# Kernel optimization log

Hardware: AMD Instinct MI355X
Metric: run time of the kernel (lower is better)

The kernel has to match this reference:

```python
import jax, jax.numpy as jnp
import numpy as np

D_MODEL = 512
N_HEADS = 8
D_KV = 64
INNER = N_HEADS * D_KV
NUM_BUCKETS = 32
MAX_DISTANCE = 128
LN_EPS = 1e-6


def _relative_position_bucket(rel, num_buckets=NUM_BUCKETS, max_distance=MAX_DISTANCE):
    # bidirectional T5 bucketing
    nb = num_buckets // 2
    buckets = (rel > 0).astype(jnp.int32) * nb
    rel = jnp.abs(rel)
    max_exact = nb // 2
    is_small = rel < max_exact
    relf = jnp.maximum(rel.astype(jnp.float32), 1.0)  # guard log(0)
    large = max_exact + (
        jnp.log(relf / max_exact) / np.log(max_distance / max_exact) * (nb - max_exact)
    ).astype(jnp.int32)
    large = jnp.minimum(large, nb - 1)
    return buckets + jnp.where(is_small, rel, large)


def t5_layer_norm(x, weight, eps=LN_EPS):
    # T5 LayerNorm: no mean subtraction, no bias
    var = jnp.mean(jnp.square(x), axis=-1, keepdims=True)
    return x * jax.lax.rsqrt(var + eps) * weight


def compute_position_bias(rel_bias_table, q_len, k_len):
    ctx = jnp.arange(q_len)[:, None]
    mem = jnp.arange(k_len)[None, :]
    buckets = _relative_position_bucket(mem - ctx)  # [q, k]
    bias = rel_bias_table[buckets]                  # [q, k, H]
    return jnp.transpose(bias, (2, 0, 1))[None]     # [1, H, q, k]


def setup_inputs() -> dict:
    key = jax.random.key(0)
    ks = jax.random.split(key, 8)
    N, S = 8, 2048
    s = 1.0 / np.sqrt(D_MODEL)
    return {
        "hidden_states": jax.random.normal(ks[0], (N, S, D_MODEL), jnp.float32),
        "ln_weight": jnp.ones((D_MODEL,), jnp.float32),
        "wq": jax.random.normal(ks[1], (D_MODEL, INNER), jnp.float32) * s,
        "wk": jax.random.normal(ks[2], (D_MODEL, INNER), jnp.float32) * s,
        "wv": jax.random.normal(ks[3], (D_MODEL, INNER), jnp.float32) * s,
        "wo": jax.random.normal(ks[4], (INNER, D_MODEL), jnp.float32) * s,
        "rel_bias_table": jax.random.normal(ks[5], (NUM_BUCKETS, N_HEADS), jnp.float32) * 0.1,
        "seq_idx2graph_idx": jax.random.randint(ks[6], (8,), 0, 8, jnp.int64) if jax.config.jax_enable_x64 else jax.random.randint(ks[6], (8,), 0, 8, jnp.int32),
    }


def reference(hidden_states, ln_weight, wq, wk, wv, wo, rel_bias_table, seq_idx2graph_idx):
    N, S, _ = hidden_states.shape
    normed = t5_layer_norm(hidden_states, ln_weight)

    # T5Attention (no 1/sqrt(d) scaling in T5)
    q = jnp.einsum("nsd,de->nse", normed, wq).reshape(N, S, N_HEADS, D_KV)
    k = jnp.einsum("nsd,de->nse", normed, wk).reshape(N, S, N_HEADS, D_KV)
    v = jnp.einsum("nsd,de->nse", normed, wv).reshape(N, S, N_HEADS, D_KV)

    position_bias = compute_position_bias(rel_bias_table, S, S)  # [1,H,S,S]
    scores = jnp.einsum("nqhd,nkhd->nhqk", q, k) + position_bias
    attn = jax.nn.softmax(scores, axis=-1)
    ctx = jnp.einsum("nhqk,nkhd->nqhd", attn, v).reshape(N, S, INNER)
    attn_out = jnp.einsum("nse,ed->nsd", ctx, wo)

    # residual (dropout is identity in eval)
    hidden = hidden_states + attn_out
    remain_node_idx = jnp.arange(seq_idx2graph_idx.shape[0])
    return hidden, position_bias, remain_node_idx
```

## Files before the change

kernel.cpp:

```cpp
#include <hip/hip_runtime.h>
#include <hip/hip_bf16.h>
#include <math.h>

typedef __bf16 bf16;
typedef bf16 bf16x8 __attribute__((ext_vector_type(8)));
typedef bf16 bf16x4 __attribute__((ext_vector_type(4)));
typedef float f32x2 __attribute__((ext_vector_type(2)));
typedef float f32x4 __attribute__((ext_vector_type(4)));
typedef float f32x16 __attribute__((ext_vector_type(16)));

#define MFMA16(a, b, c) __builtin_amdgcn_mfma_f32_16x16x32_bf16(a, b, c, 0, 0, 0)
#define MFMA32(a, b, c) __builtin_amdgcn_mfma_f32_32x32x16_bf16(a, b, c, 0, 0, 0)
#define LOG2E 1.4426950408889634f
#define NEG_SHIFT -40.0f

__device__ __forceinline__ void glds16(const bf16* g, bf16* l) {
  __builtin_amdgcn_global_load_lds(
      (const __attribute__((address_space(1))) void*)g,
      (__attribute__((address_space(3))) void*)l, 16, 0, 0);
}

__device__ inline unsigned pkbf(float a, float b) {
  union { bf16 h; unsigned short u; } ca, cb;
  ca.h = (bf16)a;
  cb.h = (bf16)b;
  return (unsigned)ca.u | ((unsigned)cb.u << 16);
}

__device__ __forceinline__ void pl32swap(unsigned& a, unsigned& b) {
  asm("v_permlane32_swap_b32 %0, %1" : "+v"(a), "+v"(b));
}

__device__ inline float t5bias(const float* __restrict__ table, int h, int x) {
  if (x > 4094) return 0.f;
  int rel = x - 2047;
  int bucket = (rel > 0) ? 16 : 0;
  int ar = rel < 0 ? -rel : rel;
  int v;
  if (ar < 8) {
    v = ar;
  } else {
    double tt = log((double)ar / 8.0) / log(16.0) * 8.0;
    int lg = 8 + (int)tt;
    v = lg < 15 ? lg : 15;
  }
  return table[(bucket + v) * 8 + h];
}

__global__ __launch_bounds__(256) void prep_kernel(
    const float* __restrict__ hidden, const float* __restrict__ ln_w,
    const float* __restrict__ wq, const float* __restrict__ wk,
    const float* __restrict__ wv, const float* __restrict__ wo,
    const float* __restrict__ table, bf16* __restrict__ normed,
    float* __restrict__ lut, float4* __restrict__ lutq,
    float* __restrict__ out_remain, bf16* __restrict__ wt_qkv,
    bf16* __restrict__ wt_o) {
  __shared__ float tile[32][33];
  int bid = blockIdx.x;
  int t = threadIdx.x;
  if (bid < 4096) {
    int row = bid * 4 + (t >> 6);
    int lane = t & 63;
    const float4* xr = (const float4*)(hidden + (size_t)row * 512);
    float4 a = xr[lane];
    float4 b = xr[lane + 64];
    float s = a.x * a.x + a.y * a.y + a.z * a.z + a.w * a.w +
              b.x * b.x + b.y * b.y + b.z * b.z + b.w * b.w;
#pragma unroll
    for (int off = 32; off > 0; off >>= 1) s += __shfl_down(s, off, 64);
    float tot = __shfl(s, 0, 64);
    float rscale = rsqrtf(tot * (1.0f / 512.0f) + 1e-6f);
    float4 w0 = *(const float4*)(ln_w + 4 * lane);
    float4 w1 = *(const float4*)(ln_w + 256 + 4 * lane);
    bf16x4 o0, o1;
    o0[0] = (bf16)(a.x * rscale * w0.x);
    o0[1] = (bf16)(a.y * rscale * w0.y);
    o0[2] = (bf16)(a.z * rscale * w0.z);
    o0[3] = (bf16)(a.w * rscale * w0.w);
    o1[0] = (bf16)(b.x * rscale * w1.x);
    o1[1] = (bf16)(b.y * rscale * w1.y);
    o1[2] = (bf16)(b.z * rscale * w1.z);
    o1[3] = (bf16)(b.w * rscale * w1.w);
    *(bf16x4*)(normed + (size_t)row * 512 + 4 * lane) = o0;
    *(bf16x4*)(normed + (size_t)row * 512 + 256 + 4 * lane) = o1;
  } else if (bid < 4224) {
    int i = (bid - 4096) * 256 + t;
    int h = i >> 12;
    int d = i & 4095;
    lut[(size_t)h * 4096 + d] = t5bias(table, h, d);
    if (i < 8) out_remain[i] = (float)i;
  } else if (bid < 5248) {
    int bid2 = bid - 4224;
    int mat = bid2 >> 8;
    int rem = bid2 & 255;
    int e0 = (rem & 15) * 32;
    int k0 = (rem >> 4) * 32;
    int tx = t & 31, ty = t >> 5;
    const float* W = (mat == 0) ? wq : (mat == 1) ? wk : (mat == 2) ? wv : wo;
#pragma unroll
    for (int j = 0; j < 32; j += 8)
      tile[ty + j][tx] = W[(size_t)(k0 + ty + j) * 512 + e0 + tx];
    __syncthreads();
    bf16* dst = (mat < 3) ? (wt_qkv + (size_t)mat * 512 * 512) : wt_o;
#pragma unroll
    for (int j = 0; j < 32; j += 8)
      dst[(size_t)(e0 + ty + j) * 512 + k0 + tx] = (bf16)tile[tx][ty + j];
  } else {
    int i = (bid - 5248) * 256 + t;
    int h = i >> 12;
    int d = i & 4095;
    float4 o;
    o.x = t5bias(table, h, d) * LOG2E + NEG_SHIFT;
    o.y = t5bias(table, h, d + 1) * LOG2E + NEG_SHIFT;
    o.z = t5bias(table, h, d + 2) * LOG2E + NEG_SHIFT;
    o.w = t5bias(table, h, d + 3) * LOG2E + NEG_SHIFT;
    lutq[(size_t)h * 4096 + d] = o;
  }
}

__global__ __launch_bounds__(256) void qkv_gemm(
    const bf16* __restrict__ normed, const bf16* __restrict__ wt,
    bf16* __restrict__ qb, bf16* __restrict__ kb, bf16* __restrict__ vtb) {
  __shared__ __align__(16) char smem[19456];
  bf16* As = (bf16*)smem;
  bf16* Bs = (bf16*)(smem + 8192);
  int t = threadIdx.x;
  int wave = t >> 6, lane = t & 63;
  int quad = lane >> 4, lc = lane & 15;
  int wm = wave >> 1, wn = wave & 1;
  int m0 = blockIdx.x * 128, n0 = blockIdx.y * 128;

  f32x4 acc[4][4];
#pragma unroll
  for (int i = 0; i < 4; i++)
#pragma unroll
    for (int j = 0; j < 4; j++) acc[i][j] = (f32x4){0.f, 0.f, 0.f, 0.f};

  int rw = lane >> 2;
  int c8 = (lane & 3) * 8;
  const bf16* gA = normed + (size_t)(m0 + wave * 32 + rw) * 512 + c8;
  const bf16* gB = wt + (size_t)(n0 + wave * 32 + rw) * 512 + c8;
  bf16* lA = As + wave * 1024;
  bf16* lB = Bs + wave * 1024;

  for (int kt = 0; kt < 16; ++kt) {
    int k0 = kt * 32;
    __syncthreads();
    glds16(gA + k0, lA);
    glds16(gA + 16 * 512 + k0, lA + 512);
    glds16(gB + k0, lB);
    glds16(gB + 16 * 512 + k0, lB + 512);
    __syncthreads();
    bf16x8 af[4], bfr[4];
#pragma unroll
    for (int i = 0; i < 4; i++)
      af[i] = *(const bf16x8*)&As[(wm * 64 + i * 16 + lc) * 32 + quad * 8];
#pragma unroll
    for (int j = 0; j < 4; j++)
      bfr[j] = *(const bf16x8*)&Bs[(wn * 64 + j * 16 + lc) * 32 + quad * 8];
#pragma unroll
    for (int i = 0; i < 4; i++)
#pragma unroll
      for (int j = 0; j < 4; j++)
        acc[i][j] = MFMA16(af[i], bfr[j], acc[i][j]);
  }

  __syncthreads();
  int mat = n0 >> 9;
  int e_base = (n0 & 511) + wn * 64;
  int hh = e_base >> 6;
  int grow0 = m0 + wm * 64;
  int nbi = grow0 >> 11, sbase = grow0 & 2047;

  if (mat == 2) {
    bf16* dv = vtb + ((size_t)(nbi * 8 + hh) * 64) * 2048;
#pragma unroll
    for (int i = 0; i < 4; i++) {
      int s = sbase + i * 16 + quad * 4;
#pragma unroll
      for (int j = 0; j < 4; j++) {
        int d = j * 16 + lc;
        bf16x4 o4;
#pragma unroll
        for (int r = 0; r < 4; r++) o4[r] = (bf16)acc[i][j][r];
        *(bf16x4*)(dv + (size_t)d * 2048 + s) = o4;
      }
    }
  } else {
    float qsc = (mat == 0) ? LOG2E : 1.0f;
    bf16* dst0 = (mat == 0) ? qb : kb;
    bf16* dst = dst0 + (((size_t)nbi * 8 + hh) * 2048 + sbase) * 64;
    bf16* Cw = (bf16*)smem + wave * 2432;
#pragma unroll
    for (int p = 0; p < 2; ++p) {
#pragma unroll
      for (int i2 = 0; i2 < 2; ++i2) {
#pragma unroll
        for (int j = 0; j < 4; ++j)
#pragma unroll
          for (int r = 0; r < 4; ++r)
            Cw[(i2 * 16 + quad * 4 + r) * 76 + j * 16 + lc] =
                (bf16)(acc[2 * p + i2][j][r] * qsc);
      }
#pragma unroll
      for (int c = 0; c < 4; ++c) {
        bf16x8 vch =
            *(const bf16x8*)&Cw[(c * 8 + (lane >> 3)) * 76 + (lane & 7) * 8];
        *(bf16x8*)(dst + (size_t)(p * 32 + c * 8 + (lane >> 3)) * 64 +
                   (lane & 7) * 8) = vch;
      }
    }
  }
}

#define LDB4(SV, G, V4)       \
  {                           \
    float4 _b = (V4);         \
    SV[4 * (G) + 0] = _b.x;   \
    SV[4 * (G) + 1] = _b.y;   \
    SV[4 * (G) + 2] = _b.z;   \
    SV[4 * (G) + 3] = _b.w;   \
  }

#define BODY(RB, WB, PF)                                                     \
  {                                                                          \
    if (PF) {                                                                \
      kv0 = *(const bf16x8*)(kpc);                                           \
      kv1 = *(const bf16x8*)(kpc + 8);                                       \
      vv0 = *(const bf16x8*)(vpc);                                           \
      vv1 = *(const bf16x8*)(vpc + 8);                                       \
    }                                                                        \
    _Pragma("unroll") for (int mi = 0; mi < 2; mi++) {                       \
      __builtin_amdgcn_s_setprio(1);                                         \
      _Pragma("unroll") for (int c = 0; c < 4; c++) {                        \
        bf16x8 kf = *(const bf16x8*)&Ks[RB][mi * 32 + l31][c * 16 + hi * 8]; \
        st[mi] = MFMA32(kf, Qf[c], st[mi]);                                  \
      }                                                                      \
      __builtin_amdgcn_s_setprio(0);                                         \
      unsigned D[8];                                                         \
      _Pragma("unroll") for (int g = 0; g < 4; g++) {                        \
        _Pragma("unroll") for (int e = 0; e < 4; e++)                        \
            st[mi][4 * g + e] = __builtin_amdgcn_exp2f(st[mi][4 * g + e]);   \
        lsA += (f32x2){st[mi][4 * g + 0], st[mi][4 * g + 1]};                \
        lsB += (f32x2){st[mi][4 * g + 2], st[mi][4 * g + 3]};                \
        D[2 * g] = pkbf(st[mi][4 * g + 0], st[mi][4 * g + 1]);               \
        D[2 * g + 1] = pkbf(st[mi][4 * g + 2], st[mi][4 * g + 3]);           \
      }                                                                      \
      if (PF) {         \
        LDB4(st[mi], 0, bpn[mi * 32 + 0]);                                   \
        LDB4(st[mi], 1, bpn[mi * 32 + 8]);                                   \
        LDB4(st[mi], 2, bpn[mi * 32 + 16]);                                  \
        LDB4(st[mi], 3, bpn[mi * 32 + 24]);                                  \
      }                                                                      \
      pl32swap(D[0], D[2]);                                                  \
      pl32swap(D[1], D[3]);                                                  \
      pl32swap(D[4], D[6]);                                                  \
      pl32swap(D[5], D[7]);                                                  \
      _Pragma("unroll") for (int kk = 0; kk < 2; kk++) {                     \
        int kc = 2 * mi + kk;                                                \
        union { uint4 u; bf16x8 v; } cv;                                     \
        cv.u = make_uint4(D[4 * kk + 0], D[4 * kk + 1], D[4 * kk + 2],       \
                          D[4 * kk + 3]);                                    \
        bf16x8 pf = cv.v;                                                    \
        __builtin_amdgcn_s_setprio(1);                                       \
        _Pragma("unroll") for (int md = 0; md < 2; md++) {                   \
          bf16x8 vf =                                                        \
              *(const bf16x8*)&Vs[RB][md * 32 + l31][kc * 16 + hi * 8];      \
          O[md] = MFMA32(vf, pf, O[md]);                                     \
        }                                                                    \
        __builtin_amdgcn_s_setprio(0);                                       \
      }                                                                      \
    }                                                                        \
    if (PF) {                                                                \
      *(bf16x8*)&Ks[WB][srow][scol] = kv0;                                   \
      *(bf16x8*)&Ks[WB][srow][scol + 8] = kv1;                               \
      *(bf16x8*)&Vs[WB][srow][scol] = vv0;                                   \
      *(bf16x8*)&Vs[WB][srow][scol + 8] = vv1;                               \
      kpc += 4096;                                                           \
      vpc += 64;                                                             \
      bpn += 64;                                                             \
    }                                                                        \
    __syncthreads();                                                         \
  }

__global__ __launch_bounds__(256, 4) void attn_kernel(
    const bf16* __restrict__ qg, const bf16* __restrict__ kg,
    const bf16* __restrict__ vtg, const float4* __restrict__ lutq,
    bf16* __restrict__ ctx) {
  __shared__ bf16 Ks[2][64][72];
  __shared__ bf16 Vs[2][64][72];
  int t = threadIdx.x;

  int id = blockIdx.x;
  int xcd = id & 7, slot = id >> 3;
  int bh = xcd * 8 + (slot >> 4);
  int qt = slot & 15;
  int n = bh >> 3, h = bh & 7;
  int q0 = qt * 128;

  int wave = t >> 6, lane = t & 63;
  int l31 = lane & 31, hi = lane >> 5;
  int q = q0 + wave * 32 + l31;

  const float4* bp = lutq + (size_t)h * 4096 + (2047 + 4 * hi - q);

  const bf16* qp = qg + ((size_t)bh * 2048 + q) * 64;
  bf16x8 Qf[4];
#pragma unroll
  for (int c = 0; c < 4; c++) Qf[c] = *(const bf16x8*)(qp + c * 16 + hi * 8);

  f32x16 O[2];
#pragma unroll
  for (int i = 0; i < 2; i++)
#pragma unroll
    for (int e = 0; e < 16; e++) O[i][e] = 0.f;
  f32x2 lsA = {0.f, 0.f}, lsB = {0.f, 0.f};

  int srow = t >> 2, scol = (t & 3) * 16;
  const bf16* kp = kg + (size_t)bh * 2048 * 64 + srow * 64 + scol;
  const bf16* vp = vtg + (size_t)bh * 64 * 2048 + (size_t)srow * 2048 + scol;

  bf16x8 kv0 = *(const bf16x8*)(kp);
  bf16x8 kv1 = *(const bf16x8*)(kp + 8);
  bf16x8 vv0 = *(const bf16x8*)(vp);
  bf16x8 vv1 = *(const bf16x8*)(vp + 8);
  *(bf16x8*)&Ks[0][srow][scol] = kv0;
  *(bf16x8*)&Ks[0][srow][scol + 8] = kv1;
  *(bf16x8*)&Vs[0][srow][scol] = vv0;
  *(bf16x8*)&Vs[0][srow][scol + 8] = vv1;
  f32x16 st[2];
  LDB4(st[0], 0, bp[0]);
  LDB4(st[0], 1, bp[8]);
  LDB4(st[0], 2, bp[16]);
  LDB4(st[0], 3, bp[24]);
  LDB4(st[1], 0, bp[32]);
  LDB4(st[1], 1, bp[40]);
  LDB4(st[1], 2, bp[48]);
  LDB4(st[1], 3, bp[56]);
  const bf16* kpc = kp + 4096;
  const bf16* vpc = vp + 64;
  const float4* bpn = bp + 64;
  __syncthreads();

#pragma unroll 1
  for (int it = 0; it < 15; ++it) {
    BODY(0, 1, 1)
    BODY(1, 0, 1)
  }
  BODY(0, 1, 1)
  BODY(1, 0, 0)

  float l_run = lsA.x + lsA.y + lsB.x + lsB.y;
  l_run += __shfl_xor(l_run, 32, 64);
  float inv = 1.0f / l_run;
  bf16* cp = ctx + ((size_t)n * 2048 + q) * 512 + h * 64;
#pragma unroll
  for (int md = 0; md < 2; md++)
#pragma unroll
    for (int g = 0; g < 4; g++) {
      bf16x4 o4;
#pragma unroll
      for (int e = 0; e < 4; e++) o4[e] = (bf16)(O[md][4 * g + e] * inv);
      *(bf16x4*)(cp + md * 32 + 8 * g + hi * 4) = o4;
    }
}

__global__ __launch_bounds__(256) void oproj_gemm(
    const bf16* __restrict__ ctx, const bf16* __restrict__ wt_o,
    const float* __restrict__ hidden, float* __restrict__ out,
    const float* __restrict__ lut, float* __restrict__ bias_out) {
  __shared__ __align__(16) char smem[16384];
  int t = threadIdx.x;
  int bid = blockIdx.x;

  if (bid >= 512) {
    int bb = bid - 512;
#pragma unroll
    for (int j = 0; j < 4; ++j) {
      size_t i = ((size_t)bb * 1024 + j * 256 + t) * 4;
      int h = (int)(i >> 22);
      int q = (int)((i >> 11) & 2047);
      int k = (int)(i & 2047);
      const float* lh = lut + (size_t)h * 4096 + (2047 - q);
      float4 v = {lh[k], lh[k + 1], lh[k + 2], lh[k + 3]};
      *(float4*)(bias_out + i) = v;
    }
    return;
  }

  bf16* As = (bf16*)smem;
  bf16* Bs = (bf16*)(smem + 8192);
  int wave = t >> 6, lane = t & 63;
  int quad = lane >> 4, lc = lane & 15;
  int wm = wave >> 1, wn = wave & 1;
  int m0 = (bid & 127) * 128, n0 = (bid >> 7) * 128;

  f32x4 acc[4][4];
#pragma unroll
  for (int i = 0; i < 4; i++)
#pragma unroll
    for (int j = 0; j < 4; j++) acc[i][j] = (f32x4){0.f, 0.f, 0.f, 0.f};

  int rw = lane >> 2;
  int c8 = (lane & 3) * 8;
  const bf16* gA = ctx + (size_t)(m0 + wave * 32 + rw) * 512 + c8;
  const bf16* gB = wt_o + (size_t)(n0 + wave * 32 + rw) * 512 + c8;
  bf16* lA = As + wave * 1024;
  bf16* lB = Bs + wave * 1024;

  for (int kt = 0; kt < 16; ++kt) {
    int k0 = kt * 32;
    __syncthreads();
    glds16(gA + k0, lA);
    glds16(gA + 16 * 512 + k0, lA + 512);
    glds16(gB + k0, lB);
    glds16(gB + 16 * 512 + k0, lB + 512);
    __syncthreads();
    bf16x8 af[4], bfr[4];
#pragma unroll
    for (int i = 0; i < 4; i++)
      af[i] = *(const bf16x8*)&As[(wm * 64 + i * 16 + lc) * 32 + quad * 8];
#pragma unroll
    for (int j = 0; j < 4; j++)
      bfr[j] = *(const bf16x8*)&Bs[(wn * 64 + j * 16 + lc) * 32 + quad * 8];
#pragma unroll
    for (int i = 0; i < 4; i++)
#pragma unroll
      for (int j = 0; j < 4; j++)
        acc[i][j] = MFMA16(af[i], bfr[j], acc[i][j]);
  }

#pragma unroll
  for (int i = 0; i < 4; i++) {
#pragma unroll
    for (int j = 0; j < 4; j++) {
#pragma unroll
      for (int r = 0; r < 4; r++) {
        int grow = m0 + wm * 64 + i * 16 + quad * 4 + r;
        int gcol = n0 + wn * 64 + j * 16 + lc;
        size_t idx = (size_t)grow * 512 + gcol;
        out[idx] = acc[i][j][r] + hidden[idx];
      }
    }
  }
}

extern "C" void kernel_launch(void* const* d_in, const int* in_sizes, int n_in,
                              void* d_out, int out_size, void* d_ws, size_t ws_size,
                              hipStream_t stream) {
  const float* hidden = (const float*)d_in[0];
  const float* ln_w = (const float*)d_in[1];
  const float* wq = (const float*)d_in[2];
  const float* wk = (const float*)d_in[3];
  const float* wv = (const float*)d_in[4];
  const float* wo = (const float*)d_in[5];
  const float* table = (const float*)d_in[6];

  float* out_hidden = (float*)d_out;
  float* out_bias = out_hidden + (size_t)8 * 2048 * 512;
  float* out_remain = out_bias + (size_t)8 * 2048 * 2048;

  char* ws = (char*)d_ws;
  bf16* normed = (bf16*)(ws + 0);
  float* lut = (float*)(ws + 16777216);
  float4* lutq = (float4*)(ws + 16908288);
  bf16* wt_qkv = (bf16*)(ws + 17432576);
  bf16* wt_o = (bf16*)(ws + 19005440);
  bf16* qb = (bf16*)(ws + 19529728);
  bf16* kb = qb + (size_t)8 * 8 * 2048 * 64;
  bf16* vtb = kb + (size_t)8 * 8 * 2048 * 64;
  bf16* ctx = normed;

  prep_kernel<<<dim3(5376), dim3(256), 0, stream>>>(
      hidden, ln_w, wq, wk, wv, wo, table, normed, lut, lutq, out_remain,
      wt_qkv, wt_o);
  qkv_gemm<<<dim3(128, 12), dim3(256), 0, stream>>>(normed, wt_qkv, qb, kb, vtb);
  attn_kernel<<<dim3(1024), dim3(256), 0, stream>>>(qb, kb, vtb, lutq, ctx);
  oproj_gemm<<<dim3(512 + 8192), dim3(256), 0, stream>>>(ctx, wt_o, hidden,
                                                         out_hidden, lut,
                                                         out_bias);
}
```

Baseline: 380.4 us.

## Load K/V fragments directly from global memory and fuse bias write into attention

The attention kernel drops its LDS double-buffering of K and V tiles. Each wave now loads its MFMA operand fragments straight from global memory, relying on L1/L2 reuse across waves instead of shared memory and barriers. The separate position-bias materialization blocks move out of the output-projection launch and into the tail of each attention block, so the 128MB bias write overlaps attention work. This removes the syncthreads and LDS traffic, but each wave now issues redundant global loads and depends on cache hit rates.

```diff
diff --git a/kernel.cpp b/kernel.cpp
--- a/kernel.cpp
+++ b/kernel.cpp
@@ -222,75 +222,12 @@
     SV[4 * (G) + 3] = _b.w;   \
   }
 
-#define BODY(RB, WB, PF)                                                     \
-  {                                                                          \
-    if (PF) {                                                                \
-      kv0 = *(const bf16x8*)(kpc);                                           \
-      kv1 = *(const bf16x8*)(kpc + 8);                                       \
-      vv0 = *(const bf16x8*)(vpc);                                           \
-      vv1 = *(const bf16x8*)(vpc + 8);                                       \
-    }                                                                        \
-    _Pragma("unroll") for (int mi = 0; mi < 2; mi++) {                       \
-      __builtin_amdgcn_s_setprio(1);                                         \
-      _Pragma("unroll") for (int c = 0; c < 4; c++) {                        \
-        bf16x8 kf = *(const bf16x8*)&Ks[RB][mi * 32 + l31][c * 16 + hi * 8]; \
-        st[mi] = MFMA32(kf, Qf[c], st[mi]);                                  \
-      }                                                                      \
-      __builtin_amdgcn_s_setprio(0);                                         \
-      unsigned D[8];                                                         \
-      _Pragma("unroll") for (int g = 0; g < 4; g++) {                        \
-        _Pragma("unroll") for (int e = 0; e < 4; e++)                        \
-            st[mi][4 * g + e] = __builtin_amdgcn_exp2f(st[mi][4 * g + e]);   \
-        lsA += (f32x2){st[mi][4 * g + 0], st[mi][4 * g + 1]};                \
-        lsB += (f32x2){st[mi][4 * g + 2], st[mi][4 * g + 3]};                \
-        D[2 * g] = pkbf(st[mi][4 * g + 0], st[mi][4 * g + 1]);               \
-        D[2 * g + 1] = pkbf(st[mi][4 * g + 2], st[mi][4 * g + 3]);           \
-      }                                                                      \
-      if (PF) {         \
-        LDB4(st[mi], 0, bpn[mi * 32 + 0]);                                   \
-        LDB4(st[mi], 1, bpn[mi * 32 + 8]);                                   \
-        LDB4(st[mi], 2, bpn[mi * 32 + 16]);                                  \
-        LDB4(st[mi], 3, bpn[mi * 32 + 24]);                                  \
-      }                                                                      \
-      pl32swap(D[0], D[2]);                                                  \
-      pl32swap(D[1], D[3]);                                                  \
-      pl32swap(D[4], D[6]);                                                  \
-      pl32swap(D[5], D[7]);                                                  \
-      _Pragma("unroll") for (int kk = 0; kk < 2; kk++) {                     \
-        int kc = 2 * mi + kk;                                                \
-        union { uint4 u; bf16x8 v; } cv;                                     \
-        cv.u = make_uint4(D[4 * kk + 0], D[4 * kk + 1], D[4 * kk + 2],       \
-                          D[4 * kk + 3]);                                    \
-        bf16x8 pf = cv.v;                                                    \
-        __builtin_amdgcn_s_setprio(1);                                       \
-        _Pragma("unroll") for (int md = 0; md < 2; md++) {                   \
-          bf16x8 vf =                                                        \
-              *(const bf16x8*)&Vs[RB][md * 32 + l31][kc * 16 + hi * 8];      \
-          O[md] = MFMA32(vf, pf, O[md]);                                     \
-        }                                                                    \
-        __builtin_amdgcn_s_setprio(0);                                       \
-      }                                                                      \
-    }                                                                        \
-    if (PF) {                                                                \
-      *(bf16x8*)&Ks[WB][srow][scol] = kv0;                                   \
-      *(bf16x8*)&Ks[WB][srow][scol + 8] = kv1;                               \
-      *(bf16x8*)&Vs[WB][srow][scol] = vv0;                                   \
-      *(bf16x8*)&Vs[WB][srow][scol + 8] = vv1;                               \
-      kpc += 4096;                                                           \
-      vpc += 64;                                                             \
-      bpn += 64;                                                             \
-    }                                                                        \
-    __syncthreads();                                                         \
-  }
-
 __global__ __launch_bounds__(256, 4) void attn_kernel(
     const bf16* __restrict__ qg, const bf16* __restrict__ kg,
     const bf16* __restrict__ vtg, const float4* __restrict__ lutq,
-    bf16* __restrict__ ctx) {
-  __shared__ bf16 Ks[2][64][72];
-  __shared__ bf16 Vs[2][64][72];
+    const float* __restrict__ lut, bf16* __restrict__ ctx,
+    float* __restrict__ bias_out) {
   int t = threadIdx.x;
-
   int id = blockIdx.x;
   int xcd = id & 7, slot = id >> 3;
   int bh = xcd * 8 + (slot >> 4);
@@ -309,6 +246,10 @@
 #pragma unroll
   for (int c = 0; c < 4; c++) Qf[c] = *(const bf16x8*)(qp + c * 16 + hi * 8);
 
+  const bf16* kbase = kg + (size_t)bh * 2048 * 64 + (size_t)l31 * 64 + hi * 8;
+  const bf16* vbase =
+      vtg + (size_t)bh * 64 * 2048 + (size_t)l31 * 2048 + hi * 8;
+
   f32x16 O[2];
 #pragma unroll
   for (int i = 0; i < 2; i++)
@@ -316,18 +257,6 @@
     for (int e = 0; e < 16; e++) O[i][e] = 0.f;
   f32x2 lsA = {0.f, 0.f}, lsB = {0.f, 0.f};
 
-  int srow = t >> 2, scol = (t & 3) * 16;
-  const bf16* kp = kg + (size_t)bh * 2048 * 64 + srow * 64 + scol;
-  const bf16* vp = vtg + (size_t)bh * 64 * 2048 + (size_t)srow * 2048 + scol;
-
-  bf16x8 kv0 = *(const bf16x8*)(kp);
-  bf16x8 kv1 = *(const bf16x8*)(kp + 8);
-  bf16x8 vv0 = *(const bf16x8*)(vp);
-  bf16x8 vv1 = *(const bf16x8*)(vp + 8);
-  *(bf16x8*)&Ks[0][srow][scol] = kv0;
-  *(bf16x8*)&Ks[0][srow][scol + 8] = kv1;
-  *(bf16x8*)&Vs[0][srow][scol] = vv0;
-  *(bf16x8*)&Vs[0][srow][scol + 8] = vv1;
   f32x16 st[2];
   LDB4(st[0], 0, bp[0]);
   LDB4(st[0], 1, bp[8]);
@@ -337,18 +266,62 @@
   LDB4(st[1], 1, bp[40]);
   LDB4(st[1], 2, bp[48]);
   LDB4(st[1], 3, bp[56]);
-  const bf16* kpc = kp + 4096;
-  const bf16* vpc = vp + 64;
   const float4* bpn = bp + 64;
-  __syncthreads();
 
 #pragma unroll 1
-  for (int it = 0; it < 15; ++it) {
-    BODY(0, 1, 1)
-    BODY(1, 0, 1)
-  }
-  BODY(0, 1, 1)
-  BODY(1, 0, 0)
+  for (int kt = 0; kt < 32; ++kt) {
+    const bf16* kT = kbase + (size_t)kt * 4096;
+    const bf16* vT = vbase + kt * 64;
+    bool pf = (kt < 31);
+#pragma unroll
+    for (int mi = 0; mi < 2; mi++) {
+      bf16x8 kf0 = *(const bf16x8*)(kT + mi * 2048);
+      bf16x8 kf1 = *(const bf16x8*)(kT + mi * 2048 + 16);
+      bf16x8 kf2 = *(const bf16x8*)(kT + mi * 2048 + 32);
+      bf16x8 kf3 = *(const bf16x8*)(kT + mi * 2048 + 48);
+      __builtin_amdgcn_s_setprio(1);
+      st[mi] = MFMA32(kf0, Qf[0], st[mi]);
+      st[mi] = MFMA32(kf1, Qf[1], st[mi]);
+      st[mi] = MFMA32(kf2, Qf[2], st[mi]);
+      st[mi] = MFMA32(kf3, Qf[3], st[mi]);
+      __builtin_amdgcn_s_setprio(0);
+      bf16x8 vf00 = *(const bf16x8*)(vT + (2 * mi) * 16);
+      bf16x8 vf01 = *(const bf16x8*)(vT + 65536 + (2 * mi) * 16);
+      bf16x8 vf10 = *(const bf16x8*)(vT + (2 * mi + 1) * 16);
+      bf16x8 vf11 = *(const bf16x8*)(vT + 65536 + (2 * mi + 1) * 16);
+      unsigned D[8];
+#pragma unroll
+      for (int g = 0; g < 4; g++) {
+#pragma unroll
+        for (int e = 0; e < 4; e++)
+          st[mi][4 * g + e] = __builtin_amdgcn_exp2f(st[mi][4 * g + e]);
+        lsA += (f32x2){st[mi][4 * g + 0], st[mi][4 * g + 1]};
+        lsB += (f32x2){st[mi][4 * g + 2], st[mi][4 * g + 3]};
+        D[2 * g] = pkbf(st[mi][4 * g + 0], st[mi][4 * g + 1]);
+        D[2 * g + 1] = pkbf(st[mi][4 * g + 2], st[mi][4 * g + 3]);
+      }
+      if (pf) {
+        LDB4(st[mi], 0, bpn[mi * 32 + 0]);
+        LDB4(st[mi], 1, bpn[mi * 32 + 8]);
+        LDB4(st[mi], 2, bpn[mi * 32 + 16]);
+        LDB4(st[mi], 3, bpn[mi * 32 + 24]);
+      }
+      pl32swap(D[0], D[2]);
+      pl32swap(D[1], D[3]);
+      pl32swap(D[4], D[6]);
+      pl32swap(D[5], D[7]);
+      union { uint4 u; bf16x8 v; } cv0, cv1;
+      cv0.u = make_uint4(D[0], D[1], D[2], D[3]);
+      cv1.u = make_uint4(D[4], D[5], D[6], D[7]);
+      __builtin_amdgcn_s_setprio(1);
+      O[0] = MFMA32(vf00, cv0.v, O[0]);
+      O[1] = MFMA32(vf01, cv0.v, O[1]);
+      O[0] = MFMA32(vf10, cv1.v, O[0]);
+      O[1] = MFMA32(vf11, cv1.v, O[1]);
+      __builtin_amdgcn_s_setprio(0);
+    }
+    if (pf) bpn += 64;
+  }
 
   float l_run = lsA.x + lsA.y + lsB.x + lsB.y;
   l_run += __shfl_xor(l_run, 32, 64);
@@ -363,37 +336,32 @@
       for (int e = 0; e < 4; e++) o4[e] = (bf16)(O[md][4 * g + e] * inv);
       *(bf16x4*)(cp + md * 32 + 8 * g + hi * 4) = o4;
     }
+
+  int qbase = qt * 128 + n * 16;
+  const float* lbase = lut + (size_t)h * 4096;
+  float* bout = bias_out + ((size_t)h * 2048 + qbase) * 2048;
+#pragma unroll 2
+  for (int jj = 0; jj < 32; ++jj) {
+    int L = jj * 256 + t;
+    int r = L >> 9;
+    int c4 = L & 511;
+    const float* lh = lbase + (2047 - (qbase + r)) + c4 * 4;
+    float4 v = {lh[0], lh[1], lh[2], lh[3]};
+    *(float4*)(bout + (size_t)r * 2048 + c4 * 4) = v;
+  }
 }
 
 __global__ __launch_bounds__(256) void oproj_gemm(
     const bf16* __restrict__ ctx, const bf16* __restrict__ wt_o,
-    const float* __restrict__ hidden, float* __restrict__ out,
-    const float* __restrict__ lut, float* __restrict__ bias_out) {
+    const float* __restrict__ hidden, float* __restrict__ out) {
   __shared__ __align__(16) char smem[16384];
-  int t = threadIdx.x;
-  int bid = blockIdx.x;
-
-  if (bid >= 512) {
-    int bb = bid - 512;
-#pragma unroll
-    for (int j = 0; j < 4; ++j) {
-      size_t i = ((size_t)bb * 1024 + j * 256 + t) * 4;
-      int h = (int)(i >> 22);
-      int q = (int)((i >> 11) & 2047);
-      int k = (int)(i & 2047);
-      const float* lh = lut + (size_t)h * 4096 + (2047 - q);
-      float4 v = {lh[k], lh[k + 1], lh[k + 2], lh[k + 3]};
-      *(float4*)(bias_out + i) = v;
-    }
-    return;
-  }
-
   bf16* As = (bf16*)smem;
   bf16* Bs = (bf16*)(smem + 8192);
+  int t = threadIdx.x;
   int wave = t >> 6, lane = t & 63;
   int quad = lane >> 4, lc = lane & 15;
   int wm = wave >> 1, wn = wave & 1;
-  int m0 = (bid & 127) * 128, n0 = (bid >> 7) * 128;
+  int m0 = blockIdx.x * 128, n0 = blockIdx.y * 128;
 
   f32x4 acc[4][4];
 #pragma unroll
@@ -475,8 +443,8 @@
       hidden, ln_w, wq, wk, wv, wo, table, normed, lut, lutq, out_remain,
       wt_qkv, wt_o);
   qkv_gemm<<<dim3(128, 12), dim3(256), 0, stream>>>(normed, wt_qkv, qb, kb, vtb);
-  attn_kernel<<<dim3(1024), dim3(256), 0, stream>>>(qb, kb, vtb, lutq, ctx);
-  oproj_gemm<<<dim3(512 + 8192), dim3(256), 0, stream>>>(ctx, wt_o, hidden,
-                                                         out_hidden, lut,
-                                                         out_bias);
-}
+  attn_kernel<<<dim3(1024), dim3(256), 0, stream>>>(qb, kb, vtb, lutq, lut, ctx,
+                                                    out_bias);
+  oproj_gemm<<<dim3(128, 4), dim3(256), 0, stream>>>(ctx, wt_o, hidden,
+                                                     out_hidden);
+}
```

Result: slower. 628.4 us (+65.2%).
